# Kernel tuning notes

Measured on AMD Instinct MI355X. Metric: run time of the kernel, lower is better.

The kernel has to match this reference:

```python
import jax, jax.numpy as jnp
import numpy as np

H = 96  # hidden_dim


def _rbf(dist):
    # GaussianSmearing(start=0, stop=10, num_gaussians=16)
    offset = jnp.linspace(0.0, 10.0, 16, dtype=dist.dtype)
    coeff = -0.5 / (10.0 / 15.0) ** 2
    d = dist[:, None] - offset[None, :]
    return jnp.exp(coeff * d * d)


def _gatv2(s, edge, edge_attr, Wl, bl, Wr, br, We, att, bias):
    # PyG GATv2Conv, heads=1: e = leaky_relu(lin_l(x_src)+lin_r(x_tgt)+lin_edge(ea));
    # alpha = segment_softmax(e @ att, tgt); out = scatter_sum(alpha * lin_l(x_src)) + bias
    N = s.shape[0]
    src, tgt = edge[0], edge[1]
    xl = s @ Wl + bl
    xr = s @ Wr + br
    e = jax.nn.leaky_relu(xl[src] + xr[tgt] + edge_attr @ We, 0.2)  # [E,H]
    logits = e @ att  # [E]
    m = jax.ops.segment_max(logits, tgt, num_segments=N)
    a = jnp.exp(logits - m[tgt])
    denom = jax.ops.segment_sum(a, tgt, num_segments=N)
    alpha = a / denom[tgt]
    out = jax.ops.segment_sum(alpha[:, None] * xl[src], tgt, num_segments=N)
    return out + bias


def _encoder(x, edge, pos, Wemb, bemb, gp):
    s0 = x @ Wemb + bemb                      # [N,H]
    s = jax.nn.silu(s0)
    row, col = edge[0], edge[1]
    dist = jnp.linalg.norm(pos[row] - pos[col], axis=-1)
    ea = _rbf(dist)                           # [E,16]
    s = s + jax.nn.silu(_gatv2(s, edge, ea, *gp))
    v = s0.reshape(x.shape[0], -1, 3)[:, :16, :]  # [N,16,3]
    return s, v


def _forward(x_L, pos_L, x_P, pos_P, edge_L, edge_P, cross_src, cross_tgt,
             Wemb_L, bemb_L, Wl_L, bl_L, Wr_L, br_L, We_L, att_L, bias_L,
             Wemb_P, bemb_P, Wl_P, bl_P, Wr_P, br_P, We_P, att_P, bias_P,
             Win, b_in, Wout, bout, Wq, bq, Wk, bk, Wv, bv, W1, b1, W2, b2):
    s_L, v_L = _encoder(x_L, edge_L, pos_L, Wemb_L, bemb_L,
                        (Wl_L, bl_L, Wr_L, br_L, We_L, att_L, bias_L))
    s_P, v_P = _encoder(x_P, edge_P, pos_P, Wemb_P, bemb_P,
                        (Wl_P, bl_P, Wr_P, br_P, We_P, att_P, bias_P))
    # CausalMolSSM: x + out_proj(silu(in_proj(x)).chunk(2)[0])
    h = jax.nn.silu(s_L @ Win + b_in)[:, : 2 * H]
    s_L = s_L + h @ Wout + bout
    # GVPCrossAttention: per-edge gather, global softmax (dim=0 in source), scatter-add
    q = (s_L @ Wq + bq)[cross_tgt]
    k = (s_P @ Wk + bk)[cross_src]
    logits = jnp.sum(q * k, axis=-1) / 8.0     # [E_X]
    attn = jax.nn.softmax(logits, axis=0)      # global softmax over all edges (as in source)
    vmsg = (s_P @ Wv + bv)[cross_src]
    s_L = s_L.at[cross_tgt].add(attn[:, None] * vmsg)
    # head
    return jax.nn.silu(s_L @ W1 + b1) @ W2 + b2  # v_pred [N_L,3]


def setup_inputs() -> dict:
    N_L, N_P = 8192, 32768
    E_L, E_P, E_X = 262144, 524288, 262144
    D_L, D_P = 167, 21
    ks = iter(jax.random.split(jax.random.key(0), 64))

    def w(shape, fan):
        return (jax.random.normal(next(ks), shape, dtype=jnp.float32) / np.sqrt(fan)).astype(jnp.float32)

    inp = {}
    inp['x_L'] = jax.random.normal(next(ks), (N_L, D_L), dtype=jnp.float32)
    inp['pos_L'] = jax.random.normal(next(ks), (N_L, 3), dtype=jnp.float32)
    inp['x_P'] = jax.random.normal(next(ks), (N_P, D_P), dtype=jnp.float32)
    inp['pos_P'] = jax.random.normal(next(ks), (N_P, 3), dtype=jnp.float32)
    inp['edge_L'] = jax.random.randint(next(ks), (2, E_L), 0, N_L)
    inp['edge_P'] = jax.random.randint(next(ks), (2, E_P), 0, N_P)
    inp['cross_src'] = jax.random.randint(next(ks), (E_X,), 0, N_P)
    inp['cross_tgt'] = jax.random.randint(next(ks), (E_X,), 0, N_L)
    for pre, din in (('L', D_L), ('P', D_P)):
        inp[f'Wemb_{pre}'] = w((din, H), din); inp[f'bemb_{pre}'] = w((H,), din)
        inp[f'Wl_{pre}'] = w((H, H), H); inp[f'bl_{pre}'] = w((H,), H)
        inp[f'Wr_{pre}'] = w((H, H), H); inp[f'br_{pre}'] = w((H,), H)
        inp[f'We_{pre}'] = w((16, H), 16)
        inp[f'att_{pre}'] = w((H,), H)
        inp[f'bias_{pre}'] = w((H,), H)
    inp['Win'] = w((H, 4 * H), H); inp['b_in'] = w((4 * H,), H)
    inp['Wout'] = w((2 * H, H), 2 * H); inp['bout'] = w((H,), 2 * H)
    for n in ('q', 'k', 'v'):
        inp[f'W{n}'] = w((H, H), H); inp[f'b{n}'] = w((H,), H)
    inp['W1'] = w((H, H), H); inp['b1'] = w((H,), H)
    inp['W2'] = w((H, 3), H); inp['b2'] = w((3,), H)
    return inp


def reference(x_L, pos_L, x_P, pos_P, edge_L, edge_P, cross_src, cross_tgt,
              Wemb_L, bemb_L, Wl_L, bl_L, Wr_L, br_L, We_L, att_L, bias_L,
              Wemb_P, bemb_P, Wl_P, bl_P, Wr_P, br_P, We_P, att_P, bias_P,
              Win, b_in, Wout, bout, Wq, bq, Wk, bk, Wv, bv, W1, b1, W2, b2):
    return _forward(x_L, pos_L, x_P, pos_P, edge_L, edge_P, cross_src, cross_tgt,
                    Wemb_L, bemb_L, Wl_L, bl_L, Wr_L, br_L, We_L, att_L, bias_L,
                    Wemb_P, bemb_P, Wl_P, bl_P, Wr_P, br_P, We_P, att_P, bias_P,
                    Win, b_in, Wout, bout, Wq, bq, Wk, bk, Wv, bv, W1, b1, W2, b2)
```

## Files before the change

kernel.cpp:

```cpp
#include <hip/hip_runtime.h>

__device__ __forceinline__ float silu_f(float x) { return x / (1.f + __expf(-x)); }

__device__ __forceinline__ void atomicMaxF(float* addr, float val) {
    if (val >= 0.f) atomicMax((int*)addr, __float_as_int(val));
    else            atomicMin((unsigned int*)addr, __float_as_uint(val));
}

__device__ __forceinline__ unsigned short f2bf(float x) {
    unsigned int u = __float_as_uint(x);
    return (unsigned short)((u + 0x7fffu + ((u >> 16) & 1u)) >> 16);
}
__device__ __forceinline__ float bf2f(unsigned short h) {
    return __uint_as_float(((unsigned int)h) << 16);
}
__device__ __forceinline__ float bf_lo(unsigned int u) { return __uint_as_float(u << 16); }
__device__ __forceinline__ float bf_hi(unsigned int u) { return __uint_as_float(u & 0xffff0000u); }
__device__ __forceinline__ float bfdot(unsigned int a, unsigned int b) {
    return bf_lo(a) * bf_lo(b) + bf_hi(a) * bf_hi(b);
}

__global__ void fill_i(int* __restrict__ p, int v, int n) {
    int i = blockIdx.x * blockDim.x + threadIdx.x;
    if (i < n) p[i] = v;
}

__global__ __launch_bounds__(256) void hist_all_kernel(const int* __restrict__ tgtL,
        const int* __restrict__ tgtP, const int* __restrict__ ctgt, int* __restrict__ count,
        int E_L, int E_P, int E_X, int N_L, int N_P) {
    int e = blockIdx.x * blockDim.x + threadIdx.x;
    if (e < E_L) atomicAdd(&count[tgtL[e]], 1);
    else if (e < E_L + E_P) atomicAdd(&count[N_L + tgtP[e - E_L]], 1);
    else if (e < E_L + E_P + E_X) atomicAdd(&count[N_L + N_P + ctgt[e - E_L - E_P]], 1);
}

__global__ __launch_bounds__(256) void scan_blocksum_kernel(const int* __restrict__ count,
                                                            int* __restrict__ bsum, int n) {
    int b = blockIdx.x, t = threadIdx.x;
    int base = b * 4096 + t * 16;
    int s = 0;
#pragma unroll
    for (int k = 0; k < 16; ++k) {
        int idx = base + k;
        s += (idx < n) ? count[idx] : 0;
    }
#pragma unroll
    for (int off = 1; off < 64; off <<= 1) s += __shfl_xor(s, off, 64);
    __shared__ int ws[4];
    int lane = t & 63, wid = t >> 6;
    if (lane == 0) ws[wid] = s;
    __syncthreads();
    if (t == 0) bsum[b] = ws[0] + ws[1] + ws[2] + ws[3];
}

__global__ void scan_top_kernel(int* __restrict__ bsum, int nb, float* __restrict__ csc) {
    if (threadIdx.x == 0) {
        int run = 0;
        for (int i = 0; i < nb; ++i) { int c = bsum[i]; bsum[i] = run; run += c; }
        csc[0] = -3.4e38f; csc[1] = 0.f;
    }
}

__global__ __launch_bounds__(256) void scan_apply_kernel(const int* __restrict__ count,
        const int* __restrict__ bsum, int* __restrict__ rowptr, int* __restrict__ cursor,
        int n, int E) {
    int b = blockIdx.x, t = threadIdx.x;
    int base = b * 4096 + t * 16;
    int v[16];
    int s = 0;
#pragma unroll
    for (int k = 0; k < 16; ++k) {
        int idx = base + k;
        v[k] = (idx < n) ? count[idx] : 0;
        s += v[k];
    }
    int lane = t & 63, wid = t >> 6;
    int inc = s;
#pragma unroll
    for (int off = 1; off < 64; off <<= 1) {
        int o = __shfl_up(inc, off, 64);
        if (lane >= off) inc += o;
    }
    __shared__ int ws[4];
    if (lane == 63) ws[wid] = inc;
    __syncthreads();
    int woff = 0;
    for (int w = 0; w < wid; ++w) woff += ws[w];
    int prefix = bsum[b] + woff + (inc - s);
#pragma unroll
    for (int k = 0; k < 16; ++k) {
        int idx = base + k;
        if (idx < n) { rowptr[idx] = prefix; cursor[idx] = prefix; prefix += v[k]; }
    }
    if (b == 0 && t == 0) rowptr[n] = E;
}

__global__ __launch_bounds__(256) void pre_all_kernel(const int* __restrict__ eL,
        const int* __restrict__ eP, const int* __restrict__ csrc, const int* __restrict__ ctgt,
        const float* __restrict__ posL, const float* __restrict__ posP,
        int* __restrict__ cursor, unsigned int* __restrict__ sdp,
        int E_L, int E_P, int E_X, int N_L, int N_P) {
    int e = blockIdx.x * blockDim.x + threadIdx.x;
    if (e >= E_L + E_P + E_X) return;
    unsigned int pack;
    int node;
    if (e < E_L + E_P) {
        const int* ed; const float* pos; int idx, E, nbase;
        if (e < E_L) { ed = eL; pos = posL; idx = e; E = E_L; nbase = 0; }
        else         { ed = eP; pos = posP; idx = e - E_L; E = E_P; nbase = N_L; }
        int si = ed[idx], ti = ed[E + idx];
        node = nbase + ti;
        float dx = pos[si * 3 + 0] - pos[ti * 3 + 0];
        float dy = pos[si * 3 + 1] - pos[ti * 3 + 1];
        float dz = pos[si * 3 + 2] - pos[ti * 3 + 2];
        float dist = sqrtf(dx * dx + dy * dy + dz * dz);
        int dq = min((int)(dist * 4096.f), 65535);
        pack = (unsigned int)(si + nbase) | ((unsigned int)dq << 16);
    } else {
        int idx = e - E_L - E_P;
        int ti = ctgt[idx];
        pack = (unsigned int)csrc[idx] | ((unsigned int)ti << 16);
        node = N_L + N_P + ti;
    }
    int p = atomicAdd(&cursor[node], 1);
    sdp[p] = pack;
}

__global__ __launch_bounds__(96) void rbf_table_pack_kernel(const float* __restrict__ We_L,
        const float* __restrict__ We_P, unsigned int* __restrict__ T2_L,
        unsigned int* __restrict__ T2_P) {
    int b = blockIdx.x;
    const float* We = (b < 1024) ? We_L : We_P;
    unsigned int* T2 = (b < 1024) ? T2_L : T2_P;
    int i = (b < 1024) ? b : b - 1024;
    int h = threadIdx.x;
    float d0 = (float)i * 0.015625f, d1 = (float)(i + 1) * 0.015625f;
    float a0 = 0.f, a1 = 0.f;
#pragma unroll
    for (int g = 0; g < 16; ++g) {
        float w = We[g * 96 + h];
        float t0 = d0 - 0.66666667f * (float)g;
        float t1 = d1 - 0.66666667f * (float)g;
        a0 += __expf(-1.125f * t0 * t0) * w;
        a1 += __expf(-1.125f * t1 * t1) * w;
    }
    T2[i * 96 + h] = (unsigned int)f2bf(a0) | ((unsigned int)f2bf(a1 - a0) << 16);
}

__global__ __launch_bounds__(256) void gat_all_kernel(const int* __restrict__ rowptr,
        const unsigned int* __restrict__ sdp, const unsigned short* __restrict__ xlb,
        const unsigned short* __restrict__ xrb,
        const unsigned int* __restrict__ T2_L, const unsigned int* __restrict__ T2_P,
        const float* __restrict__ att_L, const float* __restrict__ att_P,
        const float* __restrict__ bias_L, const float* __restrict__ bias_P,
        float* __restrict__ s_L, float* __restrict__ s_P, int N_L, int Ncomb) {
    int tid = threadIdx.x;
    int l = tid & 31;
    int n = blockIdx.x * 8 + (tid >> 5);
    if (n >= Ncomb) return;
    bool isL = n < N_L;
    const unsigned int* T2 = isL ? T2_L : T2_P;
    const float* att = isL ? att_L : att_P;
    const float* bias = isL ? bias_L : bias_P;
    float* srow = isL ? (s_L + (size_t)n * 96) : (s_P + (size_t)(n - N_L) * 96);
    float att0 = att[l], att1 = att[32 + l], att2 = att[64 + l];
    size_t nb = (size_t)n * 96;
    float xr0 = bf2f(xrb[nb + l]), xr1 = bf2f(xrb[nb + 32 + l]), xr2 = bf2f(xrb[nb + 64 + l]);
    int beg = rowptr[n], end = rowptr[n + 1];
    float m = -3.4e38f, d = 0.f, a0 = 0.f, a1 = 0.f, a2 = 0.f;
    for (int j = beg; j < end; j += 4) {
        unsigned int tp0[4], tp1[4], tp2[4];
        unsigned short xs0[4], xs1[4], xs2[4];
        float ff[4];
#pragma unroll
        for (int k = 0; k < 4; ++k) {
            int jj = min(j + k, end - 1);
            unsigned int u = sdp[jj];
            int src = (int)(u & 0xffffu);
            int dq = (int)(u >> 16);
            int i = dq >> 6;
            ff[k] = (float)(dq & 63) * 0.015625f;
            const unsigned int* tr = T2 + (size_t)i * 96;
            tp0[k] = tr[l]; tp1[k] = tr[32 + l]; tp2[k] = tr[64 + l];
            const unsigned short* xp = xlb + (size_t)src * 96;
            xs0[k] = xp[l]; xs1[k] = xp[32 + l]; xs2[k] = xp[64 + l];
        }
        float y0[4], y1[4], y2[4], lt[4];
#pragma unroll
        for (int k = 0; k < 4; ++k) {
            y0[k] = bf2f(xs0[k]); y1[k] = bf2f(xs1[k]); y2[k] = bf2f(xs2[k]);
            float v0 = y0[k] + xr0 + bf_lo(tp0[k]) + ff[k] * bf_hi(tp0[k]);
            float v1 = y1[k] + xr1 + bf_lo(tp1[k]) + ff[k] * bf_hi(tp1[k]);
            float v2 = y2[k] + xr2 + bf_lo(tp2[k]) + ff[k] * bf_hi(tp2[k]);
            v0 = fmaxf(v0, 0.f) + 0.2f * fminf(v0, 0.f);
            v1 = fmaxf(v1, 0.f) + 0.2f * fminf(v1, 0.f);
            v2 = fmaxf(v2, 0.f) + 0.2f * fminf(v2, 0.f);
            float t = v0 * att0 + v1 * att1 + v2 * att2;
#pragma unroll
            for (int off = 1; off < 32; off <<= 1) t += __shfl_xor(t, off, 64);
            lt[k] = (j + k < end) ? t : -3.4e38f;
        }
        float bm = fmaxf(fmaxf(lt[0], lt[1]), fmaxf(lt[2], lt[3]));
        float nm = fmaxf(m, bm);
        float sc = __expf(m - nm);
        d *= sc; a0 *= sc; a1 *= sc; a2 *= sc;
#pragma unroll
        for (int k = 0; k < 4; ++k) {
            float w = __expf(lt[k] - nm);
            d += w;
            a0 += w * y0[k]; a1 += w * y1[k]; a2 += w * y2[k];
        }
        m = nm;
    }
    float agg0 = (d > 0.f) ? a0 / d : 0.f;
    float agg1 = (d > 0.f) ? a1 / d : 0.f;
    float agg2 = (d > 0.f) ? a2 / d : 0.f;
    srow[l]      += silu_f(agg0 + bias[l]);
    srow[32 + l] += silu_f(agg1 + bias[32 + l]);
    srow[64 + l] += silu_f(agg2 + bias[64 + l]);
}

__global__ __launch_bounds__(256) void cross_logit_e_kernel(const unsigned int* __restrict__ sdX,
        const unsigned short* __restrict__ qnb, const unsigned short* __restrict__ knb,
        float* __restrict__ clog_s, float* __restrict__ csc, int E) {
    int e = blockIdx.x * blockDim.x + threadIdx.x;
    float logit = -3.4e38f;
    if (e < E) {
        unsigned int u = sdX[e];
        int src = (int)(u & 0xffffu);
        int tgt = (int)(u >> 16);
        const uint4* q4 = (const uint4*)(qnb + (size_t)tgt * 96);
        const uint4* k4 = (const uint4*)(knb + (size_t)src * 96);
        float acc = 0.f;
#pragma unroll
        for (int i = 0; i < 12; ++i) {
            uint4 qa = q4[i], ka = k4[i];
            acc += bfdot(qa.x, ka.x) + bfdot(qa.y, ka.y) + bfdot(qa.z, ka.z) + bfdot(qa.w, ka.w);
        }
        logit = acc * 0.125f;
        clog_s[e] = logit;
    }
    __shared__ float red[256];
    red[threadIdx.x] = logit; __syncthreads();
    for (int s = 128; s > 0; s >>= 1) {
        if (threadIdx.x < s) red[threadIdx.x] = fmaxf(red[threadIdx.x], red[threadIdx.x + s]);
        __syncthreads();
    }
    if (threadIdx.x == 0) atomicMaxF(&csc[0], red[0]);
}

__global__ __launch_bounds__(256) void cross_denom_kernel(const float* __restrict__ clog_s,
                                                          float* __restrict__ csc, int E) {
    int e = blockIdx.x * blockDim.x + threadIdx.x;
    float a = 0.f;
    float mg = csc[0];
    if (e < E) a = __expf(clog_s[e] - mg);
    __shared__ float red[256];
    red[threadIdx.x] = a; __syncthreads();
    for (int s = 128; s > 0; s >>= 1) {
        if (threadIdx.x < s) red[threadIdx.x] += red[threadIdx.x + s];
        __syncthreads();
    }
    if (threadIdx.x == 0) atomicAdd(&csc[1], red[0]);
}

__global__ __launch_bounds__(256) void cross_apply_v4_kernel(const int* __restrict__ rowptr,
        const unsigned int* __restrict__ sdp, const float* __restrict__ clog_s,
        const unsigned short* __restrict__ vnb, const float* __restrict__ csc,
        float* __restrict__ sL, int N, int baseX) {
    int tid = threadIdx.x;
    int l = tid & 31;
    int n = blockIdx.x * 8 + (tid >> 5);
    if (n >= N) return;
    int beg = rowptr[n], end = rowptr[n + 1];
    if (beg == end) return;
    float M = csc[0], invD = 1.f / csc[1];
    float a0 = 0.f, a1 = 0.f, a2 = 0.f;
    for (int j = beg; j < end; j += 4) {
        unsigned short v0[4], v1[4], v2[4]; float w[4];
#pragma unroll
        for (int k = 0; k < 4; ++k) {
            int jj = min(j + k, end - 1);
            int src = (int)(sdp[jj] & 0xffffu);
            const unsigned short* vp = vnb + (size_t)src * 96;
            v0[k] = vp[l]; v1[k] = vp[32 + l]; v2[k] = vp[64 + l];
            w[k] = (j + k < end) ? __expf(clog_s[jj - baseX] - M) : 0.f;
        }
#pragma unroll
        for (int k = 0; k < 4; ++k) {
            a0 += w[k] * bf2f(v0[k]); a1 += w[k] * bf2f(v1[k]); a2 += w[k] * bf2f(v2[k]);
        }
    }
    size_t nb = (size_t)n * 96;
    sL[nb + l]      += a0 * invD;
    sL[nb + 32 + l] += a1 * invD;
    sL[nb + 64 + l] += a2 * invD;
}


__global__ __launch_bounds__(192) void enc_all_kernel(
        const float* __restrict__ x_L, const float* __restrict__ x_P,
        const float* __restrict__ WembL, const float* __restrict__ bembL,
        const float* __restrict__ WembP, const float* __restrict__ bembP,
        const float* __restrict__ WlL, const float* __restrict__ blL,
        const float* __restrict__ WrL, const float* __restrict__ brL,
        const float* __restrict__ WlP, const float* __restrict__ blP,
        const float* __restrict__ WrP, const float* __restrict__ brP,
        float* __restrict__ s_L, float* __restrict__ s_P,
        unsigned short* __restrict__ xlb, unsigned short* __restrict__ xrb,
        int N_L, int N_P, int D_L, int D_P, int BL) {
    __shared__ float xs[32 * 167];
    __shared__ unsigned short ssb[32 * 96];
    int b = blockIdx.x;
    bool isL = b < BL;
    const float* x    = isL ? x_L : x_P;
    const float* Wemb = isL ? WembL : WembP;
    const float* bemb = isL ? bembL : bembP;
    const float* Wl   = isL ? WlL : WlP;
    const float* bl   = isL ? blL : blP;
    const float* Wr   = isL ? WrL : WrP;
    const float* br   = isL ? brL : brP;
    float* sOut = isL ? s_L : s_P;
    int N = isL ? N_L : N_P;
    int D = isL ? D_L : D_P;
    int n0 = (isL ? b : b - BL) * 32;
    int cbase = isL ? 0 : N_L;
    int t = threadIdx.x;
    int hg = t % 24, h4 = hg * 4;
    int rg = t / 24;
    for (int i = t; i < 32 * D; i += 192) {
        int r = i / D, dd = i - r * D, nn = n0 + r;
        xs[i] = (nn < N) ? x[(size_t)nn * D + dd] : 0.f;
    }
    __syncthreads();
    float4 be = *(const float4*)&bemb[h4];
    float acc[4][4];
#pragma unroll
    for (int r = 0; r < 4; ++r) { acc[r][0] = be.x; acc[r][1] = be.y; acc[r][2] = be.z; acc[r][3] = be.w; }
    const float* xrow = &xs[rg * 4 * D];
    for (int dd = 0; dd < D; ++dd) {
        float4 w = *(const float4*)&Wemb[dd * 96 + h4];
#pragma unroll
        for (int r = 0; r < 4; ++r) {
            float xv = xrow[r * D + dd];
            acc[r][0] += xv * w.x; acc[r][1] += xv * w.y;
            acc[r][2] += xv * w.z; acc[r][3] += xv * w.w;
        }
    }
#pragma unroll
    for (int r = 0; r < 4; ++r) {
        int row = rg * 4 + r, nn = n0 + row;
        float4 v = make_float4(silu_f(acc[r][0]), silu_f(acc[r][1]),
                               silu_f(acc[r][2]), silu_f(acc[r][3]));
        *(ushort4*)&ssb[row * 96 + h4] = make_ushort4(f2bf(v.x), f2bf(v.y), f2bf(v.z), f2bf(v.w));
        if (nn < N) *(float4*)&sOut[(size_t)nn * 96 + h4] = v;
    }
    __syncthreads();
    float4 b1v = *(const float4*)&bl[h4];
    float4 b2v = *(const float4*)&br[h4];
    float a1[4][4], a2[4][4];
#pragma unroll
    for (int r = 0; r < 4; ++r) {
        a1[r][0] = b1v.x; a1[r][1] = b1v.y; a1[r][2] = b1v.z; a1[r][3] = b1v.w;
        a2[r][0] = b2v.x; a2[r][1] = b2v.y; a2[r][2] = b2v.z; a2[r][3] = b2v.w;
    }
    const unsigned short* srow = &ssb[rg * 4 * 96];
    for (int k = 0; k < 96; ++k) {
        float4 w1 = *(const float4*)&Wl[k * 96 + h4];
        float4 w2 = *(const float4*)&Wr[k * 96 + h4];
#pragma unroll
        for (int r = 0; r < 4; ++r) {
            float xv = bf2f(srow[r * 96 + k]);
            a1[r][0] += xv * w1.x; a1[r][1] += xv * w1.y; a1[r][2] += xv * w1.z; a1[r][3] += xv * w1.w;
            a2[r][0] += xv * w2.x; a2[r][1] += xv * w2.y; a2[r][2] += xv * w2.z; a2[r][3] += xv * w2.w;
        }
    }
#pragma unroll
    for (int r = 0; r < 4; ++r) {
        int nn = n0 + rg * 4 + r;
        if (nn < N) {
            size_t o = (size_t)(cbase + nn) * 96 + h4;
            *(ushort4*)&xlb[o] = make_ushort4(f2bf(a1[r][0]), f2bf(a1[r][1]), f2bf(a1[r][2]), f2bf(a1[r][3]));
            *(ushort4*)&xrb[o] = make_ushort4(f2bf(a2[r][0]), f2bf(a2[r][1]), f2bf(a2[r][2]), f2bf(a2[r][3]));
        }
    }
}

__global__ __launch_bounds__(192) void qkv_all_kernel(
        const float* __restrict__ s_L, const float* __restrict__ s_P,
        const float* __restrict__ Wq, const float* __restrict__ bq,
        const float* __restrict__ Wk, const float* __restrict__ bk,
        const float* __restrict__ Wv, const float* __restrict__ bv,
        unsigned short* __restrict__ qnb, unsigned short* __restrict__ knb,
        unsigned short* __restrict__ vnb, int N_L, int N_P, int BL) {
    __shared__ float xs[32 * 96];
    int b = blockIdx.x;
    bool isL = b < BL;
    const float* s = isL ? s_L : s_P;
    int N = isL ? N_L : N_P;
    int n0 = (isL ? b : b - BL) * 32;
    int t = threadIdx.x;
    int hg = t % 24, h4 = hg * 4;
    int rg = t / 24;
    for (int i = t; i < 32 * 96; i += 192) {
        int r = i / 96, c = i - r * 96, nn = n0 + r;
        xs[i] = (nn < N) ? s[(size_t)nn * 96 + c] : 0.f;
    }
    __syncthreads();
    const float* srow = &xs[rg * 4 * 96];
    if (isL) {
        float4 bb = *(const float4*)&bq[h4];
        float a1[4][4];
#pragma unroll
        for (int r = 0; r < 4; ++r) { a1[r][0] = bb.x; a1[r][1] = bb.y; a1[r][2] = bb.z; a1[r][3] = bb.w; }
        for (int k = 0; k < 96; ++k) {
            float4 w = *(const float4*)&Wq[k * 96 + h4];
#pragma unroll
            for (int r = 0; r < 4; ++r) {
                float xv = srow[r * 96 + k];
                a1[r][0] += xv * w.x; a1[r][1] += xv * w.y; a1[r][2] += xv * w.z; a1[r][3] += xv * w.w;
            }
        }
#pragma unroll
        for (int r = 0; r < 4; ++r) {
            int nn = n0 + rg * 4 + r;
            if (nn < N)
                *(ushort4*)&qnb[(size_t)nn * 96 + h4] =
                    make_ushort4(f2bf(a1[r][0]), f2bf(a1[r][1]), f2bf(a1[r][2]), f2bf(a1[r][3]));
        }
    } else {
        float4 bb1 = *(const float4*)&bk[h4];
        float4 bb2 = *(const float4*)&bv[h4];
        float a1[4][4], a2[4][4];
#pragma unroll
        for (int r = 0; r < 4; ++r) {
            a1[r][0] = bb1.x; a1[r][1] = bb1.y; a1[r][2] = bb1.z; a1[r][3] = bb1.w;
            a2[r][0] = bb2.x; a2[r][1] = bb2.y; a2[r][2] = bb2.z; a2[r][3] = bb2.w;
        }
        for (int k = 0; k < 96; ++k) {
            float4 w1 = *(const float4*)&Wk[k * 96 + h4];
            float4 w2 = *(const float4*)&Wv[k * 96 + h4];
#pragma unroll
            for (int r = 0; r < 4; ++r) {
                float xv = srow[r * 96 + k];
                a1[r][0] += xv * w1.x; a1[r][1] += xv * w1.y; a1[r][2] += xv * w1.z; a1[r][3] += xv * w1.w;
                a2[r][0] += xv * w2.x; a2[r][1] += xv * w2.y; a2[r][2] += xv * w2.z; a2[r][3] += xv * w2.w;
            }
        }
#pragma unroll
        for (int r = 0; r < 4; ++r) {
            int nn = n0 + rg * 4 + r;
            if (nn < N) {
                *(ushort4*)&knb[(size_t)nn * 96 + h4] =
                    make_ushort4(f2bf(a1[r][0]), f2bf(a1[r][1]), f2bf(a1[r][2]), f2bf(a1[r][3]));
                *(ushort4*)&vnb[(size_t)nn * 96 + h4] =
                    make_ushort4(f2bf(a2[r][0]), f2bf(a2[r][1]), f2bf(a2[r][2]), f2bf(a2[r][3]));
            }
        }
    }
}

__global__ __launch_bounds__(192) void ssm3_kernel(float* __restrict__ sL,
        const float* __restrict__ Win, const float* __restrict__ b_in,
        const float* __restrict__ Wout, const float* __restrict__ bout, int N) {
    __shared__ float row[8 * 96];
    __shared__ float u[8 * 192];
    int t = threadIdx.x;
    int n0 = blockIdx.x * 8;
    for (int i = t; i < 8 * 96; i += 192) {
        int r = i / 96, c = i - r * 96, nn = n0 + r;
        row[i] = (nn < N) ? sL[(size_t)nn * 96 + c] : 0.f;
    }
    __syncthreads();
    {
        int cg = t % 48, c4 = cg * 4;
        int rg = t / 48;
        float4 bb = *(const float4*)&b_in[c4];
        float a[2][4];
#pragma unroll
        for (int r = 0; r < 2; ++r) { a[r][0] = bb.x; a[r][1] = bb.y; a[r][2] = bb.z; a[r][3] = bb.w; }
        const float* rr = &row[rg * 2 * 96];
        for (int k = 0; k < 96; ++k) {
            float4 w = *(const float4*)&Win[k * 384 + c4];
#pragma unroll
            for (int r = 0; r < 2; ++r) {
                float xv = rr[r * 96 + k];
                a[r][0] += xv * w.x; a[r][1] += xv * w.y; a[r][2] += xv * w.z; a[r][3] += xv * w.w;
            }
        }
#pragma unroll
        for (int r = 0; r < 2; ++r) {
            int ro = rg * 2 + r;
            u[ro * 192 + c4 + 0] = silu_f(a[r][0]);
            u[ro * 192 + c4 + 1] = silu_f(a[r][1]);
            u[ro * 192 + c4 + 2] = silu_f(a[r][2]);
            u[ro * 192 + c4 + 3] = silu_f(a[r][3]);
        }
    }
    __syncthreads();
    {
        int hg = t % 24, h4 = hg * 4;
        int rg2 = t / 24;
        float4 bb = *(const float4*)&bout[h4];
        float a[4] = {bb.x, bb.y, bb.z, bb.w};
        const float* ur = &u[rg2 * 192];
        for (int j = 0; j < 192; ++j) {
            float4 w = *(const float4*)&Wout[j * 96 + h4];
            float uv = ur[j];
            a[0] += uv * w.x; a[1] += uv * w.y; a[2] += uv * w.z; a[3] += uv * w.w;
        }
        int nn = n0 + rg2;
        if (nn < N) {
            float4 rv = *(const float4*)&row[rg2 * 96 + h4];
            *(float4*)&sL[(size_t)nn * 96 + h4] =
                make_float4(rv.x + a[0], rv.y + a[1], rv.z + a[2], rv.w + a[3]);
        }
    }
}

__global__ __launch_bounds__(192) void head3_kernel(const float* __restrict__ sL,
        const float* __restrict__ W1, const float* __restrict__ b1,
        const float* __restrict__ W2, const float* __restrict__ b2,
        float* __restrict__ out, int N) {
    __shared__ float buf[32 * 96];
    __shared__ float tt[32 * 96];
    int t = threadIdx.x;
    int n0 = blockIdx.x * 32;
    for (int i = t; i < 32 * 96; i += 192) {
        int r = i / 96, c = i - r * 96, nn = n0 + r;
        buf[i] = (nn < N) ? sL[(size_t)nn * 96 + c] : 0.f;
    }
    __syncthreads();
    int hg = t % 24, h4 = hg * 4;
    int rg = t / 24;
    float4 bb = *(const float4*)&b1[h4];
    float a[4][4];
#pragma unroll
    for (int r = 0; r < 4; ++r) { a[r][0] = bb.x; a[r][1] = bb.y; a[r][2] = bb.z; a[r][3] = bb.w; }
    const float* srow = &buf[rg * 4 * 96];
    for (int k = 0; k < 96; ++k) {
        float4 w = *(const float4*)&W1[k * 96 + h4];
#pragma unroll
        for (int r = 0; r < 4; ++r) {
            float xv = srow[r * 96 + k];
            a[r][0] += xv * w.x; a[r][1] += xv * w.y; a[r][2] += xv * w.z; a[r][3] += xv * w.w;
        }
    }
#pragma unroll
    for (int r = 0; r < 4; ++r) {
        int row = rg * 4 + r;
        *(float4*)&tt[row * 96 + h4] = make_float4(silu_f(a[r][0]), silu_f(a[r][1]),
                                                   silu_f(a[r][2]), silu_f(a[r][3]));
    }
    __syncthreads();
    if (t < 96) {
        int r = t / 3, c = t - r * 3;
        float o = b2[c];
        const float* tr = &tt[r * 96];
        for (int j = 0; j < 96; ++j) o += tr[j] * W2[j * 3 + c];
        int nn = n0 + r;
        if (nn < N) out[nn * 3 + c] = o;
    }
}

static inline int cdiv(int a, int b) { return (a + b - 1) / b; }

extern "C" void kernel_launch(void* const* d_in, const int* in_sizes, int n_in,
                              void* d_out, int out_size, void* d_ws, size_t ws_size,
                              hipStream_t stream) {
    const float* x_L   = (const float*)d_in[0];
    const float* pos_L = (const float*)d_in[1];
    const float* x_P   = (const float*)d_in[2];
    const float* pos_P = (const float*)d_in[3];
    const int* edge_L = (const int*)d_in[4];
    const int* edge_P = (const int*)d_in[5];
    const int* csrc   = (const int*)d_in[6];
    const int* ctgt   = (const int*)d_in[7];
    const float *Wemb_L = (const float*)d_in[8],  *bemb_L = (const float*)d_in[9];
    const float *Wl_L = (const float*)d_in[10], *bl_L = (const float*)d_in[11];
    const float *Wr_L = (const float*)d_in[12], *br_L = (const float*)d_in[13];
    const float *We_L = (const float*)d_in[14], *att_L = (const float*)d_in[15], *bias_L = (const float*)d_in[16];
    const float *Wemb_P = (const float*)d_in[17], *bemb_P = (const float*)d_in[18];
    const float *Wl_P = (const float*)d_in[19], *bl_P = (const float*)d_in[20];
    const float *Wr_P = (const float*)d_in[21], *br_P = (const float*)d_in[22];
    const float *We_P = (const float*)d_in[23], *att_P = (const float*)d_in[24], *bias_P = (const float*)d_in[25];
    const float *Win = (const float*)d_in[26], *b_in = (const float*)d_in[27];
    const float *Wout = (const float*)d_in[28], *bout = (const float*)d_in[29];
    const float *Wq = (const float*)d_in[30], *bq = (const float*)d_in[31];
    const float *Wk = (const float*)d_in[32], *bk = (const float*)d_in[33];
    const float *Wv = (const float*)d_in[34], *bv = (const float*)d_in[35];
    const float *W1 = (const float*)d_in[36], *b1 = (const float*)d_in[37];
    const float *W2 = (const float*)d_in[38], *b2 = (const float*)d_in[39];

    const int N_L = in_sizes[1] / 3;
    const int N_P = in_sizes[3] / 3;
    const int E_L = in_sizes[4] / 2;
    const int E_P = in_sizes[5] / 2;
    const int E_X = in_sizes[6];
    const int D_L = in_sizes[0] / N_L;
    const int D_P = in_sizes[2] / N_P;
    const int Ncomb = N_L + N_P;
    const int Ntot = N_L + N_P + N_L;
    const int Etot = E_L + E_P + E_X;
    const int baseX = E_L + E_P;

    float* ws = (float*)d_ws;
    float*          s_L    = ws;
    float*          s_P    = s_L + (size_t)N_L * 96;
    unsigned short* xrb    = (unsigned short*)(s_P + (size_t)N_P * 96);
    unsigned short* xlb    = xrb + (size_t)Ncomb * 96;
    unsigned short* knb    = xlb + (size_t)Ncomb * 96;
    unsigned short* vnb    = knb + (size_t)N_P * 96;
    unsigned short* qnb    = vnb + (size_t)N_P * 96;
    unsigned int*   sdp    = (unsigned int*)(qnb + (size_t)N_L * 96);
    float*          clog_s = (float*)(sdp + (size_t)Etot);
    unsigned int*   T2_L   = (unsigned int*)(clog_s + (size_t)E_X);
    unsigned int*   T2_P   = T2_L + 1024 * 96;
    int*            rowptr = (int*)(T2_P + 1024 * 96);
    int*            count  = rowptr + (size_t)Ntot + 1;
    int*            cursor = count + (size_t)Ntot;
    float*          csc    = (float*)(cursor + (size_t)Ntot);
    int*            bsum   = (int*)(csc + 2);

    const int BL32 = cdiv(N_L, 32), BP32 = cdiv(N_P, 32);

    rbf_table_pack_kernel<<<2048, 96, 0, stream>>>(We_L, We_P, T2_L, T2_P);
    fill_i<<<cdiv(Ntot, 256), 256, 0, stream>>>(count, 0, Ntot);
    hist_all_kernel<<<cdiv(Etot, 256), 256, 0, stream>>>(edge_L + E_L, edge_P + E_P, ctgt,
        count, E_L, E_P, E_X, N_L, N_P);
    scan_blocksum_kernel<<<cdiv(Ntot, 4096), 256, 0, stream>>>(count, bsum, Ntot);
    scan_top_kernel<<<1, 64, 0, stream>>>(bsum, cdiv(Ntot, 4096), csc);
    scan_apply_kernel<<<cdiv(Ntot, 4096), 256, 0, stream>>>(count, bsum, rowptr, cursor, Ntot, Etot);
    pre_all_kernel<<<cdiv(Etot, 256), 256, 0, stream>>>(edge_L, edge_P, csrc, ctgt,
        pos_L, pos_P, cursor, sdp, E_L, E_P, E_X, N_L, N_P);

    enc_all_kernel<<<BL32 + BP32, 192, 0, stream>>>(x_L, x_P, Wemb_L, bemb_L, Wemb_P, bemb_P,
        Wl_L, bl_L, Wr_L, br_L, Wl_P, bl_P, Wr_P, br_P,
        s_L, s_P, xlb, xrb, N_L, N_P, D_L, D_P, BL32);

    gat_all_kernel<<<cdiv(Ncomb, 8), 256, 0, stream>>>(rowptr, sdp, xlb, xrb, T2_L, T2_P,
        att_L, att_P, bias_L, bias_P, s_L, s_P, N_L, Ncomb);

    ssm3_kernel<<<cdiv(N_L, 8), 192, 0, stream>>>(s_L, Win, b_in, Wout, bout, N_L);

    qkv_all_kernel<<<BL32 + BP32, 192, 0, stream>>>(s_L, s_P, Wq, bq, Wk, bk, Wv, bv,
        qnb, knb, vnb, N_L, N_P, BL32);
    cross_logit_e_kernel<<<cdiv(E_X, 256), 256, 0, stream>>>(sdp + (size_t)baseX, qnb, knb,
        clog_s, csc, E_X);
    cross_denom_kernel<<<cdiv(E_X, 256), 256, 0, stream>>>(clog_s, csc, E_X);
    cross_apply_v4_kernel<<<cdiv(N_L, 8), 256, 0, stream>>>(rowptr + N_L + N_P, sdp,
        clog_s, vnb, csc, s_L, N_L, baseX);

    head3_kernel<<<cdiv(N_L, 32), 192, 0, stream>>>(s_L, W1, b1, W2, b2, (float*)d_out, N_L);
}
```

Baseline: 469.8 us.

## Fuse SSM into QKV kernel, drop scan_top, use finer direct RBF table

Merges the SSM block and the Q projection into one kernel alongside the K/V projection. It also removes the single-thread scan_top launch by having each scan_apply block sum the preceding block totals itself, and moves the csc init into the fill kernel. The RBF lookup changes from a 1024-entry interpolated packed table to a 4096-entry direct bf16 table, which removes the interpolation arithmetic and halves the bytes per edge gathered from the table. Unroll pragmas and launch_bounds(192,1) are added to the GEMM loops. The direct table loses the interpolation term and rounds distance to a 1/256 grid, so accuracy drops slightly, and the fused Q path uses one row per thread with less register reuse.

```diff
diff --git a/kernel.cpp b/kernel.cpp
--- a/kernel.cpp
+++ b/kernel.cpp
@@ -20,9 +20,10 @@
     return bf_lo(a) * bf_lo(b) + bf_hi(a) * bf_hi(b);
 }
 
-__global__ void fill_i(int* __restrict__ p, int v, int n) {
+__global__ void fill_prep_kernel(int* __restrict__ p, int n, float* __restrict__ csc) {
     int i = blockIdx.x * blockDim.x + threadIdx.x;
-    if (i < n) p[i] = v;
+    if (i < n) p[i] = 0;
+    if (i == 0) { csc[0] = -3.4e38f; csc[1] = 0.f; }
 }
 
 __global__ __launch_bounds__(256) void hist_all_kernel(const int* __restrict__ tgtL,
@@ -53,18 +54,12 @@
     if (t == 0) bsum[b] = ws[0] + ws[1] + ws[2] + ws[3];
 }
 
-__global__ void scan_top_kernel(int* __restrict__ bsum, int nb, float* __restrict__ csc) {
-    if (threadIdx.x == 0) {
-        int run = 0;
-        for (int i = 0; i < nb; ++i) { int c = bsum[i]; bsum[i] = run; run += c; }
-        csc[0] = -3.4e38f; csc[1] = 0.f;
-    }
-}
-
 __global__ __launch_bounds__(256) void scan_apply_kernel(const int* __restrict__ count,
         const int* __restrict__ bsum, int* __restrict__ rowptr, int* __restrict__ cursor,
         int n, int E) {
     int b = blockIdx.x, t = threadIdx.x;
+    int pre = 0;
+    for (int i = 0; i < b; ++i) pre += bsum[i];
     int base = b * 4096 + t * 16;
     int v[16];
     int s = 0;
@@ -86,7 +81,7 @@
     __syncthreads();
     int woff = 0;
     for (int w = 0; w < wid; ++w) woff += ws[w];
-    int prefix = bsum[b] + woff + (inc - s);
+    int prefix = pre + woff + (inc - s);
 #pragma unroll
     for (int k = 0; k < 16; ++k) {
         int idx = base + k;
@@ -126,31 +121,28 @@
     sdp[p] = pack;
 }
 
-__global__ __launch_bounds__(96) void rbf_table_pack_kernel(const float* __restrict__ We_L,
-        const float* __restrict__ We_P, unsigned int* __restrict__ T2_L,
-        unsigned int* __restrict__ T2_P) {
+__global__ __launch_bounds__(96) void rbf_table_kernel(const float* __restrict__ We_L,
+        const float* __restrict__ We_P, unsigned short* __restrict__ T_L,
+        unsigned short* __restrict__ T_P) {
     int b = blockIdx.x;
-    const float* We = (b < 1024) ? We_L : We_P;
-    unsigned int* T2 = (b < 1024) ? T2_L : T2_P;
-    int i = (b < 1024) ? b : b - 1024;
+    const float* We = (b < 4096) ? We_L : We_P;
+    unsigned short* T = (b < 4096) ? T_L : T_P;
+    int i = (b < 4096) ? b : b - 4096;
     int h = threadIdx.x;
-    float d0 = (float)i * 0.015625f, d1 = (float)(i + 1) * 0.015625f;
-    float a0 = 0.f, a1 = 0.f;
+    float d = (float)i * 0.00390625f;
+    float a = 0.f;
 #pragma unroll
     for (int g = 0; g < 16; ++g) {
-        float w = We[g * 96 + h];
-        float t0 = d0 - 0.66666667f * (float)g;
-        float t1 = d1 - 0.66666667f * (float)g;
-        a0 += __expf(-1.125f * t0 * t0) * w;
-        a1 += __expf(-1.125f * t1 * t1) * w;
-    }
-    T2[i * 96 + h] = (unsigned int)f2bf(a0) | ((unsigned int)f2bf(a1 - a0) << 16);
+        float t = d - 0.66666667f * (float)g;
+        a += __expf(-1.125f * t * t) * We[g * 96 + h];
+    }
+    T[i * 96 + h] = f2bf(a);
 }
 
 __global__ __launch_bounds__(256) void gat_all_kernel(const int* __restrict__ rowptr,
         const unsigned int* __restrict__ sdp, const unsigned short* __restrict__ xlb,
         const unsigned short* __restrict__ xrb,
-        const unsigned int* __restrict__ T2_L, const unsigned int* __restrict__ T2_P,
+        const unsigned short* __restrict__ T_L, const unsigned short* __restrict__ T_P,
         const float* __restrict__ att_L, const float* __restrict__ att_P,
         const float* __restrict__ bias_L, const float* __restrict__ bias_P,
         float* __restrict__ s_L, float* __restrict__ s_P, int N_L, int Ncomb) {
@@ -159,7 +151,7 @@
     int n = blockIdx.x * 8 + (tid >> 5);
     if (n >= Ncomb) return;
     bool isL = n < N_L;
-    const unsigned int* T2 = isL ? T2_L : T2_P;
+    const unsigned short* T = isL ? T_L : T_P;
     const float* att = isL ? att_L : att_P;
     const float* bias = isL ? bias_L : bias_P;
     float* srow = isL ? (s_L + (size_t)n * 96) : (s_P + (size_t)(n - N_L) * 96);
@@ -169,19 +161,16 @@
     int beg = rowptr[n], end = rowptr[n + 1];
     float m = -3.4e38f, d = 0.f, a0 = 0.f, a1 = 0.f, a2 = 0.f;
     for (int j = beg; j < end; j += 4) {
-        unsigned int tp0[4], tp1[4], tp2[4];
+        unsigned short ts0[4], ts1[4], ts2[4];
         unsigned short xs0[4], xs1[4], xs2[4];
-        float ff[4];
 #pragma unroll
         for (int k = 0; k < 4; ++k) {
             int jj = min(j + k, end - 1);
             unsigned int u = sdp[jj];
             int src = (int)(u & 0xffffu);
-            int dq = (int)(u >> 16);
-            int i = dq >> 6;
-            ff[k] = (float)(dq & 63) * 0.015625f;
-            const unsigned int* tr = T2 + (size_t)i * 96;
-            tp0[k] = tr[l]; tp1[k] = tr[32 + l]; tp2[k] = tr[64 + l];
+            int i = (int)(u >> 20);
+            const unsigned short* tr = T + (size_t)i * 96;
+            ts0[k] = tr[l]; ts1[k] = tr[32 + l]; ts2[k] = tr[64 + l];
             const unsigned short* xp = xlb + (size_t)src * 96;
             xs0[k] = xp[l]; xs1[k] = xp[32 + l]; xs2[k] = xp[64 + l];
         }
@@ -189,9 +178,9 @@
 #pragma unroll
         for (int k = 0; k < 4; ++k) {
             y0[k] = bf2f(xs0[k]); y1[k] = bf2f(xs1[k]); y2[k] = bf2f(xs2[k]);
-            float v0 = y0[k] + xr0 + bf_lo(tp0[k]) + ff[k] * bf_hi(tp0[k]);
-            float v1 = y1[k] + xr1 + bf_lo(tp1[k]) + ff[k] * bf_hi(tp1[k]);
-            float v2 = y2[k] + xr2 + bf_lo(tp2[k]) + ff[k] * bf_hi(tp2[k]);
+            float v0 = y0[k] + xr0 + bf2f(ts0[k]);
+            float v1 = y1[k] + xr1 + bf2f(ts1[k]);
+            float v2 = y2[k] + xr2 + bf2f(ts2[k]);
             v0 = fmaxf(v0, 0.f) + 0.2f * fminf(v0, 0.f);
             v1 = fmaxf(v1, 0.f) + 0.2f * fminf(v1, 0.f);
             v2 = fmaxf(v2, 0.f) + 0.2f * fminf(v2, 0.f);
@@ -298,7 +287,7 @@
 }
 
 
-__global__ __launch_bounds__(192) void enc_all_kernel(
+__global__ __launch_bounds__(192, 1) void enc_all_kernel(
         const float* __restrict__ x_L, const float* __restrict__ x_P,
         const float* __restrict__ WembL, const float* __restrict__ bembL,
         const float* __restrict__ WembP, const float* __restrict__ bembP,
@@ -338,6 +327,7 @@
 #pragma unroll
     for (int r = 0; r < 4; ++r) { acc[r][0] = be.x; acc[r][1] = be.y; acc[r][2] = be.z; acc[r][3] = be.w; }
     const float* xrow = &xs[rg * 4 * D];
+#pragma unroll 4
     for (int dd = 0; dd < D; ++dd) {
         float4 w = *(const float4*)&Wemb[dd * 96 + h4];
 #pragma unroll
@@ -365,6 +355,7 @@
         a2[r][0] = b2v.x; a2[r][1] = b2v.y; a2[r][2] = b2v.z; a2[r][3] = b2v.w;
     }
     const unsigned short* srow = &ssb[rg * 4 * 96];
+#pragma unroll 4
     for (int k = 0; k < 96; ++k) {
         float4 w1 = *(const float4*)&Wl[k * 96 + h4];
         float4 w2 = *(const float4*)&Wr[k * 96 + h4];
@@ -386,49 +377,99 @@
     }
 }
 
-__global__ __launch_bounds__(192) void qkv_all_kernel(
-        const float* __restrict__ s_L, const float* __restrict__ s_P,
+__global__ __launch_bounds__(192) void ssm_qkv_kernel(
+        float* __restrict__ sL, const float* __restrict__ Win, const float* __restrict__ b_in,
+        const float* __restrict__ Wout, const float* __restrict__ bout,
         const float* __restrict__ Wq, const float* __restrict__ bq,
-        const float* __restrict__ Wk, const float* __restrict__ bk,
+        const float* __restrict__ s_P, const float* __restrict__ Wk, const float* __restrict__ bk,
         const float* __restrict__ Wv, const float* __restrict__ bv,
         unsigned short* __restrict__ qnb, unsigned short* __restrict__ knb,
-        unsigned short* __restrict__ vnb, int N_L, int N_P, int BL) {
-    __shared__ float xs[32 * 96];
+        unsigned short* __restrict__ vnb, int N_L, int N_P, int BQ) {
+    __shared__ float smem[3072];
     int b = blockIdx.x;
-    bool isL = b < BL;
-    const float* s = isL ? s_L : s_P;
-    int N = isL ? N_L : N_P;
-    int n0 = (isL ? b : b - BL) * 32;
     int t = threadIdx.x;
-    int hg = t % 24, h4 = hg * 4;
-    int rg = t / 24;
-    for (int i = t; i < 32 * 96; i += 192) {
-        int r = i / 96, c = i - r * 96, nn = n0 + r;
-        xs[i] = (nn < N) ? s[(size_t)nn * 96 + c] : 0.f;
-    }
-    __syncthreads();
-    const float* srow = &xs[rg * 4 * 96];
-    if (isL) {
-        float4 bb = *(const float4*)&bq[h4];
-        float a1[4][4];
-#pragma unroll
-        for (int r = 0; r < 4; ++r) { a1[r][0] = bb.x; a1[r][1] = bb.y; a1[r][2] = bb.z; a1[r][3] = bb.w; }
-        for (int k = 0; k < 96; ++k) {
-            float4 w = *(const float4*)&Wq[k * 96 + h4];
-#pragma unroll
-            for (int r = 0; r < 4; ++r) {
-                float xv = srow[r * 96 + k];
-                a1[r][0] += xv * w.x; a1[r][1] += xv * w.y; a1[r][2] += xv * w.z; a1[r][3] += xv * w.w;
+    if (b < BQ) {
+        float* row = smem;
+        float* u = smem + 768;
+        int n0 = b * 8;
+        for (int i = t; i < 8 * 96; i += 192) {
+            int r = i / 96, c = i - r * 96, nn = n0 + r;
+            row[i] = (nn < N_L) ? sL[(size_t)nn * 96 + c] : 0.f;
+        }
+        __syncthreads();
+        {
+            int cg = t % 48, c4 = cg * 4;
+            int rg = t / 48;
+            float4 bb = *(const float4*)&b_in[c4];
+            float a[2][4];
+#pragma unroll
+            for (int r = 0; r < 2; ++r) { a[r][0] = bb.x; a[r][1] = bb.y; a[r][2] = bb.z; a[r][3] = bb.w; }
+            const float* rr = &row[rg * 2 * 96];
+#pragma unroll 4
+            for (int k = 0; k < 96; ++k) {
+                float4 w = *(const float4*)&Win[k * 384 + c4];
+#pragma unroll
+                for (int r = 0; r < 2; ++r) {
+                    float xv = rr[r * 96 + k];
+                    a[r][0] += xv * w.x; a[r][1] += xv * w.y; a[r][2] += xv * w.z; a[r][3] += xv * w.w;
+                }
             }
-        }
-#pragma unroll
-        for (int r = 0; r < 4; ++r) {
-            int nn = n0 + rg * 4 + r;
-            if (nn < N)
+#pragma unroll
+            for (int r = 0; r < 2; ++r) {
+                int ro = rg * 2 + r;
+                u[ro * 192 + c4 + 0] = silu_f(a[r][0]);
+                u[ro * 192 + c4 + 1] = silu_f(a[r][1]);
+                u[ro * 192 + c4 + 2] = silu_f(a[r][2]);
+                u[ro * 192 + c4 + 3] = silu_f(a[r][3]);
+            }
+        }
+        __syncthreads();
+        int hg = t % 24, h4 = hg * 4;
+        int rg2 = t / 24;
+        {
+            float4 bb = *(const float4*)&bout[h4];
+            float a[4] = {bb.x, bb.y, bb.z, bb.w};
+            const float* ur = &u[rg2 * 192];
+#pragma unroll 4
+            for (int j = 0; j < 192; ++j) {
+                float4 w = *(const float4*)&Wout[j * 96 + h4];
+                float uv = ur[j];
+                a[0] += uv * w.x; a[1] += uv * w.y; a[2] += uv * w.z; a[3] += uv * w.w;
+            }
+            int nn = n0 + rg2;
+            float4 rv = *(const float4*)&row[rg2 * 96 + h4];
+            float4 fin = make_float4(rv.x + a[0], rv.y + a[1], rv.z + a[2], rv.w + a[3]);
+            if (nn < N_L) *(float4*)&sL[(size_t)nn * 96 + h4] = fin;
+            __syncthreads();
+            *(float4*)&row[rg2 * 96 + h4] = fin;
+        }
+        __syncthreads();
+        {
+            float4 bb = *(const float4*)&bq[h4];
+            float a[4] = {bb.x, bb.y, bb.z, bb.w};
+            const float* rr = &row[rg2 * 96];
+#pragma unroll 4
+            for (int k = 0; k < 96; ++k) {
+                float4 w = *(const float4*)&Wq[k * 96 + h4];
+                float xv = rr[k];
+                a[0] += xv * w.x; a[1] += xv * w.y; a[2] += xv * w.z; a[3] += xv * w.w;
+            }
+            int nn = n0 + rg2;
+            if (nn < N_L)
                 *(ushort4*)&qnb[(size_t)nn * 96 + h4] =
-                    make_ushort4(f2bf(a1[r][0]), f2bf(a1[r][1]), f2bf(a1[r][2]), f2bf(a1[r][3]));
+                    make_ushort4(f2bf(a[0]), f2bf(a[1]), f2bf(a[2]), f2bf(a[3]));
         }
     } else {
+        float* xs = smem;
+        int n0 = (b - BQ) * 32;
+        for (int i = t; i < 32 * 96; i += 192) {
+            int r = i / 96, c = i - r * 96, nn = n0 + r;
+            xs[i] = (nn < N_P) ? s_P[(size_t)nn * 96 + c] : 0.f;
+        }
+        __syncthreads();
+        int hg = t % 24, h4 = hg * 4;
+        int rg = t / 24;
+        const float* srow = &xs[rg * 4 * 96];
         float4 bb1 = *(const float4*)&bk[h4];
         float4 bb2 = *(const float4*)&bv[h4];
         float a1[4][4], a2[4][4];
@@ -437,6 +478,7 @@
             a1[r][0] = bb1.x; a1[r][1] = bb1.y; a1[r][2] = bb1.z; a1[r][3] = bb1.w;
             a2[r][0] = bb2.x; a2[r][1] = bb2.y; a2[r][2] = bb2.z; a2[r][3] = bb2.w;
         }
+#pragma unroll 4
         for (int k = 0; k < 96; ++k) {
             float4 w1 = *(const float4*)&Wk[k * 96 + h4];
             float4 w2 = *(const float4*)&Wv[k * 96 + h4];
@@ -450,70 +492,12 @@
 #pragma unroll
         for (int r = 0; r < 4; ++r) {
             int nn = n0 + rg * 4 + r;
-            if (nn < N) {
+            if (nn < N_P) {
                 *(ushort4*)&knb[(size_t)nn * 96 + h4] =
                     make_ushort4(f2bf(a1[r][0]), f2bf(a1[r][1]), f2bf(a1[r][2]), f2bf(a1[r][3]));
                 *(ushort4*)&vnb[(size_t)nn * 96 + h4] =
                     make_ushort4(f2bf(a2[r][0]), f2bf(a2[r][1]), f2bf(a2[r][2]), f2bf(a2[r][3]));
             }
-        }
-    }
-}
-
-__global__ __launch_bounds__(192) void ssm3_kernel(float* __restrict__ sL,
-        const float* __restrict__ Win, const float* __restrict__ b_in,
-        const float* __restrict__ Wout, const float* __restrict__ bout, int N) {
-    __shared__ float row[8 * 96];
-    __shared__ float u[8 * 192];
-    int t = threadIdx.x;
-    int n0 = blockIdx.x * 8;
-    for (int i = t; i < 8 * 96; i += 192) {
-        int r = i / 96, c = i - r * 96, nn = n0 + r;
-        row[i] = (nn < N) ? sL[(size_t)nn * 96 + c] : 0.f;
-    }
-    __syncthreads();
-    {
-        int cg = t % 48, c4 = cg * 4;
-        int rg = t / 48;
-        float4 bb = *(const float4*)&b_in[c4];
-        float a[2][4];
-#pragma unroll
-        for (int r = 0; r < 2; ++r) { a[r][0] = bb.x; a[r][1] = bb.y; a[r][2] = bb.z; a[r][3] = bb.w; }
-        const float* rr = &row[rg * 2 * 96];
-        for (int k = 0; k < 96; ++k) {
-            float4 w = *(const float4*)&Win[k * 384 + c4];
-#pragma unroll
-            for (int r = 0; r < 2; ++r) {
-                float xv = rr[r * 96 + k];
-                a[r][0] += xv * w.x; a[r][1] += xv * w.y; a[r][2] += xv * w.z; a[r][3] += xv * w.w;
-            }
-        }
-#pragma unroll
-        for (int r = 0; r < 2; ++r) {
-            int ro = rg * 2 + r;
-            u[ro * 192 + c4 + 0] = silu_f(a[r][0]);
-            u[ro * 192 + c4 + 1] = silu_f(a[r][1]);
-            u[ro * 192 + c4 + 2] = silu_f(a[r][2]);
-            u[ro * 192 + c4 + 3] = silu_f(a[r][3]);
-        }
-    }
-    __syncthreads();
-    {
-        int hg = t % 24, h4 = hg * 4;
-        int rg2 = t / 24;
-        float4 bb = *(const float4*)&bout[h4];
-        float a[4] = {bb.x, bb.y, bb.z, bb.w};
-        const float* ur = &u[rg2 * 192];
-        for (int j = 0; j < 192; ++j) {
-            float4 w = *(const float4*)&Wout[j * 96 + h4];
-            float uv = ur[j];
-            a[0] += uv * w.x; a[1] += uv * w.y; a[2] += uv * w.z; a[3] += uv * w.w;
-        }
-        int nn = n0 + rg2;
-        if (nn < N) {
-            float4 rv = *(const float4*)&row[rg2 * 96 + h4];
-            *(float4*)&sL[(size_t)nn * 96 + h4] =
-                make_float4(rv.x + a[0], rv.y + a[1], rv.z + a[2], rv.w + a[3]);
         }
     }
 }
@@ -538,6 +522,7 @@
 #pragma unroll
     for (int r = 0; r < 4; ++r) { a[r][0] = bb.x; a[r][1] = bb.y; a[r][2] = bb.z; a[r][3] = bb.w; }
     const float* srow = &buf[rg * 4 * 96];
+#pragma unroll 4
     for (int k = 0; k < 96; ++k) {
         float4 w = *(const float4*)&W1[k * 96 + h4];
 #pragma unroll
@@ -614,22 +599,22 @@
     unsigned short* qnb    = vnb + (size_t)N_P * 96;
     unsigned int*   sdp    = (unsigned int*)(qnb + (size_t)N_L * 96);
     float*          clog_s = (float*)(sdp + (size_t)Etot);
-    unsigned int*   T2_L   = (unsigned int*)(clog_s + (size_t)E_X);
-    unsigned int*   T2_P   = T2_L + 1024 * 96;
-    int*            rowptr = (int*)(T2_P + 1024 * 96);
+    unsigned short* T_L    = (unsigned short*)(clog_s + (size_t)E_X);
+    unsigned short* T_P    = T_L + 4096 * 96;
+    int*            rowptr = (int*)(T_P + 4096 * 96);
     int*            count  = rowptr + (size_t)Ntot + 1;
     int*            cursor = count + (size_t)Ntot;
     float*          csc    = (float*)(cursor + (size_t)Ntot);
     int*            bsum   = (int*)(csc + 2);
 
     const int BL32 = cdiv(N_L, 32), BP32 = cdiv(N_P, 32);
-
-    rbf_table_pack_kernel<<<2048, 96, 0, stream>>>(We_L, We_P, T2_L, T2_P);
-    fill_i<<<cdiv(Ntot, 256), 256, 0, stream>>>(count, 0, Ntot);
+    const int BQ = cdiv(N_L, 8);
+
+    rbf_table_kernel<<<8192, 96, 0, stream>>>(We_L, We_P, T_L, T_P);
+    fill_prep_kernel<<<cdiv(Ntot, 256), 256, 0, stream>>>(count, Ntot, csc);
     hist_all_kernel<<<cdiv(Etot, 256), 256, 0, stream>>>(edge_L + E_L, edge_P + E_P, ctgt,
         count, E_L, E_P, E_X, N_L, N_P);
     scan_blocksum_kernel<<<cdiv(Ntot, 4096), 256, 0, stream>>>(count, bsum, Ntot);
-    scan_top_kernel<<<1, 64, 0, stream>>>(bsum, cdiv(Ntot, 4096), csc);
     scan_apply_kernel<<<cdiv(Ntot, 4096), 256, 0, stream>>>(count, bsum, rowptr, cursor, Ntot, Etot);
     pre_all_kernel<<<cdiv(Etot, 256), 256, 0, stream>>>(edge_L, edge_P, csrc, ctgt,
         pos_L, pos_P, cursor, sdp, E_L, E_P, E_X, N_L, N_P);
@@ -638,13 +623,12 @@
         Wl_L, bl_L, Wr_L, br_L, Wl_P, bl_P, Wr_P, br_P,
         s_L, s_P, xlb, xrb, N_L, N_P, D_L, D_P, BL32);
 
-    gat_all_kernel<<<cdiv(Ncomb, 8), 256, 0, stream>>>(rowptr, sdp, xlb, xrb, T2_L, T2_P,
+    gat_all_kernel<<<cdiv(Ncomb, 8), 256, 0, stream>>>(rowptr, sdp, xlb, xrb, T_L, T_P,
         att_L, att_P, bias_L, bias_P, s_L, s_P, N_L, Ncomb);
 
-    ssm3_kernel<<<cdiv(N_L, 8), 192, 0, stream>>>(s_L, Win, b_in, Wout, bout, N_L);
-
-    qkv_all_kernel<<<BL32 + BP32, 192, 0, stream>>>(s_L, s_P, Wq, bq, Wk, bk, Wv, bv,
-        qnb, knb, vnb, N_L, N_P, BL32);
+    ssm_qkv_kernel<<<BQ + BP32, 192, 0, stream>>>(s_L, Win, b_in, Wout, bout, Wq, bq,
+        s_P, Wk, bk, Wv, bv, qnb, knb, vnb, N_L, N_P, BQ);
+
     cross_logit_e_kernel<<<cdiv(E_X, 256), 256, 0, stream>>>(sdp + (size_t)baseX, qnb, knb,
         clog_s, csc, E_X);
     cross_denom_kernel<<<cdiv(E_X, 256), 256, 0, stream>>>(clog_s, csc, E_X);
```

After: 473.0 us. Within noise of the previous version (+0.7%).
